# Performance work log

Hardware: AMD Instinct MI355X
Metric: run time of the kernel (lower is better)

Reference implementation:

```python
import jax, jax.numpy as jnp
import numpy as np
import math

B, T, C = 4, 2048, 1024
H = 16  # parallelAttentionPathways
D = C // H  # head dim = 64


def setup_inputs() -> dict:
    key = jax.random.key(0)
    k1, k2, k3 = jax.random.split(key, 3)
    x = jax.random.normal(k1, (B, T, C), dtype=jnp.float32)
    w_qkv = jax.random.normal(k2, (3 * C, C), dtype=jnp.float32) * (1.0 / math.sqrt(C))
    w_out = jax.random.normal(k3, (C, C), dtype=jnp.float32) * (1.0 / math.sqrt(C))
    return {"x": x, "w_qkv": w_qkv, "w_out": w_out}


def reference(x, w_qkv, w_out):
    b, t, c = x.shape
    # qkv projection: torch Linear y = x @ W^T (no bias)
    qkv = jnp.einsum('btc,fc->btf', x, w_qkv)  # [B,T,3C]
    q, k, v = jnp.split(qkv, 3, axis=-1)
    # [B,H,T,D]
    q = q.reshape(b, t, H, D).transpose(0, 2, 1, 3)
    k = k.reshape(b, t, H, D).transpose(0, 2, 1, 3)
    v = v.reshape(b, t, H, D).transpose(0, 2, 1, 3)
    scale = 1.0 / math.sqrt(D)
    att = jnp.einsum('bhqd,bhkd->bhqk', q, k) * scale  # [B,H,T,T]
    causal = jnp.tril(jnp.ones((t, t), dtype=bool))
    att = jnp.where(causal[None, None], att, -jnp.inf)
    att = jax.nn.softmax(att, axis=-1)
    # dropoutRate=0.0 -> dropout is identity (eval-mode determinism)
    y = jnp.einsum('bhqk,bhkd->bhqd', att, v)  # [B,H,T,D]
    y = y.transpose(0, 2, 1, 3).reshape(b, t, c)
    return jnp.einsum('btc,fc->btf', y, w_out)
```

## Files before the change

kernel.cpp:

```cpp
#include <hip/hip_runtime.h>
#include <hip/hip_bf16.h>
#include <stdint.h>


using bf16 = __hip_bfloat16;
typedef __attribute__((ext_vector_type(8))) __bf16 bf16x8;
typedef __attribute__((ext_vector_type(8))) unsigned short u16x8;
typedef __attribute__((ext_vector_type(4))) unsigned short u16x4;
typedef __attribute__((ext_vector_type(4))) float f32x4;
typedef unsigned short ushort_t;

#define MFMA16(a, b, c) __builtin_amdgcn_mfma_f32_16x16x32_bf16((a), (b), (c), 0, 0, 0)

__device__ __forceinline__ bf16x8 ld_frag(const ushort_t* p) {
  const u16x8 u = *(const u16x8*)p;
  return __builtin_bit_cast(bf16x8, u);
}

__device__ __forceinline__ ushort_t f2bf(float f) {
  return __builtin_bit_cast(ushort_t, __float2bfloat16(f));
}

__device__ __forceinline__ void gl2lds16(const void* g, void* lds) {
  __builtin_amdgcn_global_load_lds((const __attribute__((address_space(1))) void*)g,
                                   (__attribute__((address_space(3))) void*)lds,
                                   16, 0, 0);
}

__global__ void detect_dtype(const ushort_t* __restrict__ x, int* __restrict__ flag) {
  __shared__ int red[256];
  const int tid = threadIdx.x;
  int cnt = 0;
  for (int i = tid; i < 4096; i += 256) {
    const int e = (x[i] & 0x7FFF) >> 7;
    cnt += (e >= 117 && e <= 133) ? 1 : 0;
  }
  red[tid] = cnt;
  __syncthreads();
  for (int s = 128; s > 0; s >>= 1) {
    if (tid < s) red[tid] += red[tid + s];
    __syncthreads();
  }
  if (tid == 0) *flag = (red[0] < 3072) ? 1 : 0;
}

__global__ void cvt_to_bf16(const void* __restrict__ in, ushort_t* __restrict__ out,
                            int n, const int* __restrict__ flag) {
  const int i = (blockIdx.x * 256 + threadIdx.x) * 8;
  if (i >= n) return;
  if (*flag) {
    const float* p = (const float*)in + i;
    const float4 f0 = *(const float4*)p;
    const float4 f1 = *(const float4*)(p + 4);
    u16x8 u;
    u[0] = f2bf(f0.x); u[1] = f2bf(f0.y); u[2] = f2bf(f0.z); u[3] = f2bf(f0.w);
    u[4] = f2bf(f1.x); u[5] = f2bf(f1.y); u[6] = f2bf(f1.z); u[7] = f2bf(f1.w);
    *(u16x8*)(out + i) = u;
  } else {
    *(u16x8*)(out + i) = *(const u16x8*)((const ushort_t*)in + i);
  }
}

template <int EPI>
__global__ __launch_bounds__(256, 2)
void gemm_nt(const ushort_t* __restrict__ A, const void* __restrict__ Bw,
             const int* __restrict__ flag, int bExt,
             float* __restrict__ C0, ushort_t* __restrict__ Qo,
             ushort_t* __restrict__ Ko, ushort_t* __restrict__ Vt,
             int M, int N, int Kd) {
  __shared__ ushort_t sA[128 * 32];
  __shared__ ushort_t sB[128 * 32];
  const int tid = threadIdx.x;
  const int wave = tid >> 6, lane = tid & 63;
  const int quad = lane >> 4, l16 = lane & 15;
  const int wm = wave >> 1, wn = wave & 1;
  const long m0 = (long)blockIdx.y * 128;
  const long n0 = (long)blockIdx.x * 128;
  const int bF = bExt ? *flag : 0;

  f32x4 acc[4][4];
#pragma unroll
  for (int i = 0; i < 4; ++i)
#pragma unroll
    for (int j = 0; j < 4; ++j) acc[i][j] = (f32x4){0.f, 0.f, 0.f, 0.f};

  for (int k0 = 0; k0 < Kd; k0 += 32) {
#pragma unroll
    for (int j = 0; j < 2; ++j) {
      const int chunk = wave * 2 + j;
      const int idx = chunk * 64 + lane;
      const int r = idx >> 2, c = idx & 3;
      gl2lds16(A + (m0 + r) * (long)Kd + k0 + c * 8, (char*)sA + chunk * 1024);
    }
    if (!bF) {
#pragma unroll
      for (int j = 0; j < 2; ++j) {
        const int chunk = wave * 2 + j;
        const int idx = chunk * 64 + lane;
        const int r = idx >> 2, c = idx & 3;
        gl2lds16((const ushort_t*)Bw + (n0 + r) * (long)Kd + k0 + c * 8,
                 (char*)sB + chunk * 1024);
      }
    } else {
#pragma unroll
      for (int t2 = 0; t2 < 2; ++t2) {
        const int idx = t2 * 256 + tid;
        const int r = idx >> 2, c = idx & 3;
        const float* p = (const float*)Bw + (n0 + r) * (long)Kd + k0 + c * 8;
        const float4 f0 = *(const float4*)p;
        const float4 f1 = *(const float4*)(p + 4);
        u16x8 u;
        u[0] = f2bf(f0.x); u[1] = f2bf(f0.y); u[2] = f2bf(f0.z); u[3] = f2bf(f0.w);
        u[4] = f2bf(f1.x); u[5] = f2bf(f1.y); u[6] = f2bf(f1.z); u[7] = f2bf(f1.w);
        *(u16x8*)&sB[r * 32 + c * 8] = u;
      }
    }
    __syncthreads();
    bf16x8 af[4], bfr[4];
#pragma unroll
    for (int i = 0; i < 4; ++i) {
      const int r = wm * 64 + i * 16 + l16;
      af[i] = ld_frag(&sA[r * 32 + quad * 8]);
    }
#pragma unroll
    for (int i = 0; i < 4; ++i) {
      const int r = wn * 64 + i * 16 + l16;
      bfr[i] = ld_frag(&sB[r * 32 + quad * 8]);
    }
#pragma unroll
    for (int i = 0; i < 4; ++i)
#pragma unroll
      for (int j = 0; j < 4; ++j) acc[i][j] = MFMA16(af[i], bfr[j], acc[i][j]);
    __syncthreads();
  }

#pragma unroll
  for (int i = 0; i < 4; ++i) {
#pragma unroll
    for (int j = 0; j < 4; ++j) {
      if (EPI == 0) {
#pragma unroll
        for (int reg = 0; reg < 4; ++reg) {
          const long m = m0 + wm * 64 + i * 16 + quad * 4 + reg;
          const long n = n0 + wn * 64 + j * 16 + l16;
          C0[m * N + n] = acc[i][j][reg];
        }
      } else {
        const long n = n0 + wn * 64 + j * 16 + l16;
        const int which = (int)(n >> 10);
        const int h = (int)((n >> 6) & 15);
        const int d = (int)(n & 63);
        const long mbase = m0 + wm * 64 + i * 16 + quad * 4;
        const long b = mbase >> 11;
        const long tb = mbase & 2047;
        if (which == 2) {
          u16x4 pk;
#pragma unroll
          for (int reg = 0; reg < 4; ++reg) pk[reg] = f2bf(acc[i][j][reg]);
          *(u16x4*)&Vt[((b * 16 + h) * 64 + d) * 2048 + tb] = pk;
        } else {
          ushort_t* dst = (which == 0) ? Qo : Ko;
#pragma unroll
          for (int reg = 0; reg < 4; ++reg)
            dst[((b * 16 + h) * 2048 + tb + reg) * 64 + d] = f2bf(acc[i][j][reg]);
        }
      }
    }
  }
}


__device__ __forceinline__ void softmax_tile(f32x4* s, int kb, int qg, bool need_mask,
                                             float& m_i, float& l_i, f32x4* oacc) {
  float rmax = -1e30f;
  if (need_mask) {
#pragma unroll
    for (int nt = 0; nt < 4; ++nt) {
#pragma unroll
      for (int reg = 0; reg < 4; ++reg) {
        float v = s[nt][reg];
        if (kb + nt * 16 + reg > qg) v = -1e30f;
        s[nt][reg] = v;
        rmax = fmaxf(rmax, v);
      }
    }
  } else {
#pragma unroll
    for (int nt = 0; nt < 4; ++nt) {
#pragma unroll
      for (int reg = 0; reg < 4; ++reg) rmax = fmaxf(rmax, s[nt][reg]);
    }
  }
  rmax = fmaxf(rmax, __shfl_xor(rmax, 16, 64));
  rmax = fmaxf(rmax, __shfl_xor(rmax, 32, 64));
  float mnew = fmaxf(m_i, rmax);
  if (__all(rmax - m_i <= 5.5f)) {
    mnew = m_i;
  } else {
    const float alpha = __expf(m_i - mnew);
    l_i *= alpha;
#pragma unroll
    for (int dt = 0; dt < 4; ++dt) oacc[dt] *= alpha;
    m_i = mnew;
  }
  float rs = 0.f;
#pragma unroll
  for (int nt = 0; nt < 4; ++nt) {
#pragma unroll
    for (int reg = 0; reg < 4; ++reg) {
      const float p = __expf(s[nt][reg] - mnew);
      s[nt][reg] = p;
      rs += p;
    }
  }
  rs += __shfl_xor(rs, 16, 64);
  rs += __shfl_xor(rs, 32, 64);
  l_i += rs;
}

__device__ __forceinline__ void attn_job(const bf16x8 qf[2], const ushort_t* sKc,
                                         const ushort_t* sVc, ushort_t* sPw,
                                         int kv, int qg, bool need_mask,
                                         int quad, int l8, int l16,
                                         float& m_i, float& l_i, f32x4* oacc) {
  const f32x4 ZERO4 = {0.f, 0.f, 0.f, 0.f};
  const int off0 = ((quad ^ l8) << 3);
  const int off1 = (((quad + 4) ^ l8) << 3);
  f32x4 s[4];
#pragma unroll
  for (int nt = 0; nt < 4; ++nt) {
    const ushort_t* krow = sKc + (nt * 16 + l16) * 64;
    s[nt] = MFMA16(ld_frag(krow + off0), qf[0], ZERO4);
    s[nt] = MFMA16(ld_frag(krow + off1), qf[1], s[nt]);
  }
  softmax_tile(s, kv * 64 + quad * 4, qg, need_mask, m_i, l_i, oacc);

  asm volatile("s_waitcnt lgkmcnt(0)" ::: "memory");
#pragma unroll
  for (int nt = 0; nt < 4; ++nt) {
    u16x4 pk;
#pragma unroll
    for (int reg = 0; reg < 4; ++reg) pk[reg] = f2bf(s[nt][reg]);
    *(u16x4*)&sPw[l16 * 64 + (((4 * nt + quad) << 2) ^ (l8 << 3))] = pk;
  }
  asm volatile("s_waitcnt lgkmcnt(0)" ::: "memory");
  bf16x8 pf0 = ld_frag(&sPw[l16 * 64 + off0]);
  bf16x8 pf1 = ld_frag(&sPw[l16 * 64 + off1]);
#pragma unroll
  for (int dt = 0; dt < 4; ++dt) {
    const ushort_t* vrow = sVc + (dt * 16 + l16) * 64;
    oacc[dt] = MFMA16(ld_frag(vrow + off0), pf0, oacc[dt]);
    oacc[dt] = MFMA16(ld_frag(vrow + off1), pf1, oacc[dt]);
  }
}

__global__ __launch_bounds__(256, 4)
void attn_causal(const ushort_t* __restrict__ Qg, const ushort_t* __restrict__ Kg,
                 const ushort_t* __restrict__ Vt, ushort_t* __restrict__ Yg) {
  __shared__ ushort_t sK[2][64 * 64];
  __shared__ ushort_t sV[2][64 * 64];
  __shared__ ushort_t sP[64 * 64];
  const int tid = threadIdx.x;
  const int wave = tid >> 6, lane = tid & 63;
  const int quad = lane >> 4, l16 = lane & 15, l8 = lane & 7;
  const f32x4 ZERO4 = {0.f, 0.f, 0.f, 0.f};
  const int lin = blockIdx.y * 16 + blockIdx.x;
  const int logical = (lin & 7) * 128 + (lin >> 3);
  const int qx = logical & 15, bh = logical >> 4;
  const int qtA = qx, qtB = 31 - qx;
  const size_t base = (size_t)bh * 2048 * 64;
  ushort_t* sPw = sP + wave * 16 * 64;

  const int srow = lane >> 3;
  const int scol = ((lane & 7) ^ srow) << 3;

  bf16x8 qfA[2], qfB[2];
#pragma unroll
  for (int tile = 0; tile < 2; ++tile) {
    const int qt = tile ? qtB : qtA;
    const size_t qrow = base + (size_t)(qt * 64 + wave * 16 + l16) * 64;
#pragma unroll
    for (int kk = 0; kk < 2; ++kk) {
      const u16x8 u = *(const u16x8*)(Qg + qrow + (kk * 4 + quad) * 8);
      u16x8 w;
#pragma unroll
      for (int e = 0; e < 8; ++e)
        w[e] = f2bf(__bfloat162float(__builtin_bit_cast(bf16, (ushort_t)u[e])) * 0.125f);
      const bf16x8 f = __builtin_bit_cast(bf16x8, w);
      if (tile) qfB[kk] = f; else qfA[kk] = f;
    }
  }

  float mA = -1e30f, lA = 0.f, mB = -1e30f, lB = 0.f;
  f32x4 oA[4], oB[4];
#pragma unroll
  for (int dt = 0; dt < 4; ++dt) {
    oA[dt] = ZERO4;
    oB[dt] = ZERO4;
  }
  const int qgA = qtA * 64 + wave * 16 + l16;
  const int qgB = qtB * 64 + wave * 16 + l16;
  const int qmA = qtA * 64 + wave * 16;
  const int qmB = qtB * 64 + wave * 16;

#pragma unroll
  for (int j = 0; j < 2; ++j) {
    const int chunk = wave * 2 + j;
    gl2lds16(Kg + base + (size_t)(chunk * 8 + srow) * 64 + scol,
             (char*)&sK[0][0] + chunk * 1024);
    gl2lds16(Vt + base + (size_t)(chunk * 8 + srow) * 2048 + scol,
             (char*)&sV[0][0] + chunk * 1024);
  }

  for (int kv = 0; kv <= qtB; ++kv) {
    const int cur = kv & 1;
    __syncthreads();
    if (kv < qtB) {
      const int kn = kv + 1;
#pragma unroll
      for (int j = 0; j < 2; ++j) {
        const int chunk = wave * 2 + j;
        gl2lds16(Kg + base + (size_t)(kn * 64 + chunk * 8 + srow) * 64 + scol,
                 (char*)&sK[cur ^ 1][0] + chunk * 1024);
        gl2lds16(Vt + base + (size_t)(chunk * 8 + srow) * 2048 + kn * 64 + scol,
                 (char*)&sV[cur ^ 1][0] + chunk * 1024);
      }
    }
    const ushort_t* sKc = &sK[cur][0];
    const ushort_t* sVc = &sV[cur][0];
    attn_job(qfB, sKc, sVc, sPw, kv, qgB, kv * 64 + 63 > qmB, quad, l8, l16, mB, lB, oB);
    if (kv <= qtA)
      attn_job(qfA, sKc, sVc, sPw, kv, qgA, kv * 64 + 63 > qmA, quad, l8, l16, mA, lA, oA);
  }

  const int b = bh >> 4, h = bh & 15;
#pragma unroll
  for (int tile = 0; tile < 2; ++tile) {
    const int qt = tile ? qtB : qtA;
    const float linv = 1.f / (tile ? lB : lA);
    const f32x4* o = tile ? oB : oA;
    const int t = qt * 64 + wave * 16 + l16;
#pragma unroll
    for (int dt = 0; dt < 4; ++dt) {
      u16x4 pk;
#pragma unroll
      for (int reg = 0; reg < 4; ++reg) pk[reg] = f2bf(o[dt][reg] * linv);
      *(u16x4*)&Yg[(((size_t)b * 2048 + t) * 16 + h) * 64 + dt * 16 + quad * 4] = pk;
    }
  }
}

extern "C" void kernel_launch(void* const* d_in, const int* in_sizes, int n_in,
                              void* d_out, int out_size, void* d_ws, size_t ws_size,
                              hipStream_t stream) {
  const void* x = d_in[0];
  const void* w_qkv = d_in[1];
  const void* w_out = d_in[2];
  float* out = (float*)d_out;

  const size_t per = (size_t)4 * 16 * 2048 * 64;
  const size_t nwqkv = (size_t)3072 * 1024;
  const size_t nwout = (size_t)1024 * 1024;
  ushort_t* qws = (ushort_t*)d_ws;
  ushort_t* kws = qws + per;
  ushort_t* vTws = kws + per;
  ushort_t* xyws = vTws + per;
  ushort_t* wqkvb = xyws + per;
  ushort_t* woutb = wqkvb + nwqkv;
  int* flag = (int*)(woutb + nwout);
  const size_t need = (size_t)(4 * per + nwqkv + nwout) * 2 + 16;
  const bool pre = ws_size >= need;
  (void)in_sizes; (void)n_in; (void)out_size;

  dim3 blk(256);
  if (!pre) flag = (int*)(xyws + per);
  detect_dtype<<<1, 256, 0, stream>>>((const ushort_t*)x, flag);
  cvt_to_bf16<<<4096, 256, 0, stream>>>(x, xyws, (int)per, flag);
  if (pre) {
    cvt_to_bf16<<<1536, 256, 0, stream>>>(w_qkv, wqkvb, (int)nwqkv, flag);
    cvt_to_bf16<<<512, 256, 0, stream>>>(w_out, woutb, (int)nwout, flag);
    gemm_nt<1><<<dim3(24, 64), blk, 0, stream>>>(xyws, wqkvb, flag, 0, nullptr,
                                                 qws, kws, vTws, 8192, 3072, 1024);
    attn_causal<<<dim3(16, 64), blk, 0, stream>>>(qws, kws, vTws, xyws);
    gemm_nt<0><<<dim3(8, 64), blk, 0, stream>>>(xyws, woutb, flag, 0, out,
                                                nullptr, nullptr, nullptr,
                                                8192, 1024, 1024);
  } else {
    gemm_nt<1><<<dim3(24, 64), blk, 0, stream>>>(xyws, w_qkv, flag, 1, nullptr,
                                                 qws, kws, vTws, 8192, 3072, 1024);
    attn_causal<<<dim3(16, 64), blk, 0, stream>>>(qws, kws, vTws, xyws);
    gemm_nt<0><<<dim3(8, 64), blk, 0, stream>>>(xyws, w_out, flag, 1, out,
                                                nullptr, nullptr, nullptr,
                                                8192, 1024, 1024);
  }
}
```

Measured before the change: 264.8 us.

## Double-buffer LDS tiles in gemm_nt to overlap global loads with MFMA

Doubles the shared-memory A and B tiles and restructures the K loop so the next tile's global-to-LDS loads are issued before computing on the current tile. This replaces two __syncthreads per iteration with a single waitcnt plus barrier, so memory latency can hide behind the MFMA work. LDS use doubles to 32KB per block, which may limit occupancy under launch_bounds(256,2). The fp32-weight conversion path still loads through registers synchronously.

New measurement: 265.4 us. No clear change (+0.2%).

```diff
diff --git a/kernel.cpp b/kernel.cpp
--- a/kernel.cpp
+++ b/kernel.cpp
@@ -68,8 +68,8 @@
              float* __restrict__ C0, ushort_t* __restrict__ Qo,
              ushort_t* __restrict__ Ko, ushort_t* __restrict__ Vt,
              int M, int N, int Kd) {
-  __shared__ ushort_t sA[128 * 32];
-  __shared__ ushort_t sB[128 * 32];
+  __shared__ ushort_t sA[2][128 * 32];
+  __shared__ ushort_t sB[2][128 * 32];
   const int tid = threadIdx.x;
   const int wave = tid >> 6, lane = tid & 63;
   const int quad = lane >> 4, l16 = lane & 15;
@@ -84,14 +84,19 @@
 #pragma unroll
     for (int j = 0; j < 4; ++j) acc[i][j] = (f32x4){0.f, 0.f, 0.f, 0.f};
 
-  for (int k0 = 0; k0 < Kd; k0 += 32) {
+  const int nt = Kd >> 5;
+
+  auto stageA = [&](int buf, int k0) {
 #pragma unroll
     for (int j = 0; j < 2; ++j) {
       const int chunk = wave * 2 + j;
       const int idx = chunk * 64 + lane;
       const int r = idx >> 2, c = idx & 3;
-      gl2lds16(A + (m0 + r) * (long)Kd + k0 + c * 8, (char*)sA + chunk * 1024);
-    }
+      gl2lds16(A + (m0 + r) * (long)Kd + k0 + c * 8,
+               (char*)&sA[buf][0] + chunk * 1024);
+    }
+  };
+  auto stageB = [&](int buf, int k0) {
     if (!bF) {
 #pragma unroll
       for (int j = 0; j < 2; ++j) {
@@ -99,7 +104,7 @@
         const int idx = chunk * 64 + lane;
         const int r = idx >> 2, c = idx & 3;
         gl2lds16((const ushort_t*)Bw + (n0 + r) * (long)Kd + k0 + c * 8,
-                 (char*)sB + chunk * 1024);
+                 (char*)&sB[buf][0] + chunk * 1024);
       }
     } else {
 #pragma unroll
@@ -112,26 +117,43 @@
         u16x8 u;
         u[0] = f2bf(f0.x); u[1] = f2bf(f0.y); u[2] = f2bf(f0.z); u[3] = f2bf(f0.w);
         u[4] = f2bf(f1.x); u[5] = f2bf(f1.y); u[6] = f2bf(f1.z); u[7] = f2bf(f1.w);
-        *(u16x8*)&sB[r * 32 + c * 8] = u;
+        *(u16x8*)&sB[buf][r * 32 + c * 8] = u;
       }
     }
-    __syncthreads();
+  };
+
+  stageA(0, 0);
+  stageB(0, 0);
+  asm volatile("s_waitcnt vmcnt(0) lgkmcnt(0)" ::: "memory");
+  __builtin_amdgcn_s_barrier();
+
+  int cur = 0;
+  for (int t = 0; t < nt; ++t) {
+    if (t + 1 < nt) {
+      const int k0n = (t + 1) << 5;
+      stageA(cur ^ 1, k0n);
+      stageB(cur ^ 1, k0n);
+    }
+    const ushort_t* cA = &sA[cur][0];
+    const ushort_t* cB = &sB[cur][0];
     bf16x8 af[4], bfr[4];
 #pragma unroll
     for (int i = 0; i < 4; ++i) {
       const int r = wm * 64 + i * 16 + l16;
-      af[i] = ld_frag(&sA[r * 32 + quad * 8]);
+      af[i] = ld_frag(&cA[r * 32 + quad * 8]);
     }
 #pragma unroll
     for (int i = 0; i < 4; ++i) {
       const int r = wn * 64 + i * 16 + l16;
-      bfr[i] = ld_frag(&sB[r * 32 + quad * 8]);
+      bfr[i] = ld_frag(&cB[r * 32 + quad * 8]);
     }
 #pragma unroll
     for (int i = 0; i < 4; ++i)
 #pragma unroll
       for (int j = 0; j < 4; ++j) acc[i][j] = MFMA16(af[i], bfr[j], acc[i][j]);
-    __syncthreads();
+    asm volatile("s_waitcnt vmcnt(0) lgkmcnt(0)" ::: "memory");
+    __builtin_amdgcn_s_barrier();
+    cur ^= 1;
   }
 
 #pragma unroll
```
